# Kernel optimization log

Hardware: AMD Instinct MI355X
Metric: run time of the kernel (lower is better)

Reference implementation:

```python
import jax, jax.numpy as jnp
import numpy as np

N_HEAD = 16
MA_K = 0.02          # sigmoid temperature in ma_k_activation
LEAKY_SLOPE = 0.02   # negative_slope in ma_q_activation
NEG_INF = -1e9


def setup_inputs() -> dict:
    key = jax.random.key(0)
    k1, k2, k3, k4 = jax.random.split(key, 4)
    B, T, C = 2, 2048, 1024
    x = jax.random.normal(k1, (B, T, C), dtype=jnp.float32)
    s = 1.0 / np.sqrt(C)
    W_attn = jax.random.normal(k2, (C, 2 * C), dtype=jnp.float32) * s
    W_k2 = jax.random.normal(k3, (C, C), dtype=jnp.float32) * s
    W_proj = jax.random.normal(k4, (C, C), dtype=jnp.float32) * s
    return {"x": x, "W_attn": W_attn, "W_k2": W_k2, "W_proj": W_proj}


def _heads(t, H):
    # [B,T,C] -> [B,H,T,d]
    B, T, C = t.shape
    return t.reshape(B, T, H, C // H).transpose(0, 2, 1, 3)


def reference(x, W_attn, W_k2, W_proj):
    B, T, C = x.shape
    H = N_HEAD
    d = C // H
    scale = 1.0 / jnp.sqrt(jnp.asarray(d, x.dtype))

    qk = x @ W_attn                      # [B,T,2C]
    q, k = jnp.split(qk, 2, axis=-1)
    q = _heads(q, H)                     # [B,H,T,d]
    k = _heads(k, H)
    v = _heads(x, H)                     # v = x

    # --- AR branch: causal softmax attention ---
    scores = jnp.einsum('bhtd,bhsd->bhts', q, k) * scale
    causal = jnp.tril(jnp.ones((T, T), dtype=bool))
    scores = jnp.where(causal, scores, NEG_INF)
    attn = jax.nn.softmax(scores, axis=-1)
    y = jnp.einsum('bhts,bhsd->bhtd', attn, v)   # [B,H,T,d]

    # --- MA branch: causal, softmax-free linear attention on residual ---
    e = v[:, :, 1:, :] - y[:, :, :-1, :]          # [B,H,T-1,d]
    k2 = _heads(x[:, :-1, :] @ W_k2, H)           # [B,H,T-1,d]
    q2 = q[:, :, 1:, :]                           # [B,H,T-1,d]

    qa = -jax.nn.leaky_relu(-q2 * scale, negative_slope=LEAKY_SLOPE)
    ka = jax.nn.sigmoid(MA_K * (k2 * scale))

    w = jnp.einsum('bhtd,bhsd->bhts', qa, ka)     # [B,H,T-1,T-1]
    w = jnp.tril(w)
    y2 = jnp.einsum('bhts,bhsd->bhtd', w, e)      # [B,H,T-1,d]
    y2 = jnp.concatenate([jnp.zeros_like(y2[:, :, :1, :]), y2], axis=2)  # pad front

    def merge(t):  # [B,H,T,d] -> [B,T,C]
        return t.transpose(0, 2, 1, 3).reshape(B, T, C)

    return merge(y) @ W_proj + merge(y2) @ W_proj
```

## Files before the change

### kernel.cpp

```cpp
#include <hip/hip_runtime.h>

typedef unsigned short u16;
typedef u16   u16x4  __attribute__((ext_vector_type(4)));
typedef u16   u16x8  __attribute__((ext_vector_type(8)));
typedef __bf16 bf16x8 __attribute__((ext_vector_type(8)));
typedef float  f32x4  __attribute__((ext_vector_type(4)));

__device__ __forceinline__ float bf2f(u16 v) {
    unsigned u = ((unsigned)v) << 16;
    return __builtin_bit_cast(float, u);
}
__device__ __forceinline__ u16 f2bf(float f) {
    unsigned u = __builtin_bit_cast(unsigned, f);
    u += 0x7fffu + ((u >> 16) & 1u);
    return (u16)(u >> 16);
}

__device__ __forceinline__ size_t kimg_idx(int bh, int s, int d) {
    return ((size_t)(bh * 32 + (s >> 6)) * 4096) + (size_t)(((d >> 3) * 64 + (s & 63)) * 8) + (d & 7);
}
__device__ __forceinline__ size_t vimg_idx(int bh, int s, int d) {
    return ((size_t)(bh * 32 + (s >> 6)) * 4096) + (size_t)((((s & 63) >> 3) * 64 + d) * 8) + (s & 7);
}

__global__ __launch_bounds__(256)
void convert_pack(const float* __restrict__ in, u16* __restrict__ xb,
                  u16* __restrict__ xpack) {
    int i = blockIdx.x * 256 + threadIdx.x;
    int c4 = i & 255, row = i >> 8;
    int s = row & 2047, b = row >> 11;
    float4 v = ((const float4*)in)[i];
    u16x4 o;
    o.x = f2bf(v.x); o.y = f2bf(v.y); o.z = f2bf(v.z); o.w = f2bf(v.w);
    ((u16x4*)xb)[i] = o;
    int h = c4 >> 4, d0 = (c4 & 15) * 4;
    size_t base = vimg_idx(b * 16 + h, s, d0);
    xpack[base]      = o.x;
    xpack[base + 8]  = o.y;
    xpack[base + 16] = o.z;
    xpack[base + 24] = o.w;
}

__global__ __launch_bounds__(256)
void transpose_f32_bf16(const float* __restrict__ in, u16* __restrict__ out,
                        int R, int Cd) {
    __shared__ u16 tile[64][65];
    const int c0 = blockIdx.x * 64, r0 = blockIdx.y * 64;
    const int tid = threadIdx.x;
#pragma unroll
    for (int i = 0; i < 16; ++i) {
        int idx = tid + i * 256;
        int r = idx >> 6, c = idx & 63;
        tile[r][c] = f2bf(in[(size_t)(r0 + r) * Cd + c0 + c]);
    }
    __syncthreads();
#pragma unroll
    for (int i = 0; i < 16; ++i) {
        int idx = tid + i * 256;
        int r = idx >> 6, c = idx & 63;
        out[(size_t)(c0 + r) * R + r0 + c] = tile[c][r];
    }
}

__global__ __launch_bounds__(256, 2)
void gemm_qk(const u16* __restrict__ A, const u16* __restrict__ Bt,
             u16* __restrict__ qs, u16* __restrict__ kpack, int K) {
    __shared__ __align__(16) u16 As[4][128][8];
    __shared__ __align__(16) u16 Bs[4][128][8];
    const int tid = threadIdx.x;
    const int wave = tid >> 6, lane = tid & 63;
    const int m0 = blockIdx.y * 128, n0 = blockIdx.x * 128;
    const int wm = (wave >> 1) * 64, wn = (wave & 1) * 64;
    const int q = lane >> 4, mr = lane & 15;
    const int sr = tid >> 2, c8 = tid & 3;
    const u16* Ap = A + (size_t)(m0 + sr) * K + c8 * 8;
    const u16* Bp = Bt + (size_t)(n0 + sr) * K + c8 * 8;

    f32x4 acc[4][4];
#pragma unroll
    for (int i = 0; i < 4; ++i)
#pragma unroll
        for (int j = 0; j < 4; ++j) acc[i][j] = f32x4{0.f, 0.f, 0.f, 0.f};

    u16x8 a0, a1, b0, b1;
    auto gload = [&](int k0) {
        a0 = *(const u16x8*)(Ap + k0);
        a1 = *(const u16x8*)(Ap + k0 + (size_t)64 * K);
        b0 = *(const u16x8*)(Bp + k0);
        b1 = *(const u16x8*)(Bp + k0 + (size_t)64 * K);
    };
    gload(0);
    for (int k0 = 0; k0 < K; k0 += 32) {
        __syncthreads();
        *(u16x8*)&As[c8][sr][0]      = a0;
        *(u16x8*)&As[c8][sr + 64][0] = a1;
        *(u16x8*)&Bs[c8][sr][0]      = b0;
        *(u16x8*)&Bs[c8][sr + 64][0] = b1;
        __syncthreads();
        if (k0 + 32 < K) gload(k0 + 32);
        bf16x8 af[4], bfr[4];
#pragma unroll
        for (int i = 0; i < 4; ++i) af[i]  = *(const bf16x8*)&As[q][wm + i * 16 + mr][0];
#pragma unroll
        for (int j = 0; j < 4; ++j) bfr[j] = *(const bf16x8*)&Bs[q][wn + j * 16 + mr][0];
#pragma unroll
        for (int i = 0; i < 4; ++i)
#pragma unroll
            for (int j = 0; j < 4; ++j)
                acc[i][j] = __builtin_amdgcn_mfma_f32_16x16x32_bf16(af[i], bfr[j], acc[i][j], 0, 0, 0);
    }
#pragma unroll
    for (int i = 0; i < 4; ++i)
#pragma unroll
        for (int j = 0; j < 4; ++j)
#pragma unroll
            for (int r = 0; r < 4; ++r) {
                int m = m0 + wm + i * 16 + q * 4 + r;
                int n = n0 + wn + j * 16 + mr;
                float v = acc[i][j][r];
                if (n < 1024) {
                    qs[(size_t)m * 1024 + n] = f2bf(v * 0.125f);
                } else {
                    int b = m >> 11, s = m & 2047, nn = n - 1024;
                    kpack[kimg_idx(b * 16 + (nn >> 6), s, nn & 63)] = f2bf(v);
                }
            }
}

template <int EPI>
__global__ __launch_bounds__(256, 2)
void gemm64(const u16* __restrict__ A, const u16* __restrict__ Bt,
            void* __restrict__ Cv, int N, int K) {
    __shared__ __align__(16) u16 As[4][64][8];
    __shared__ __align__(16) u16 Bs[4][128][8];
    const int tid = threadIdx.x;
    const int wave = tid >> 6, lane = tid & 63;
    const int m0 = blockIdx.y * 64, n0 = blockIdx.x * 128;
    const int wn0 = wave * 32;
    const int q = lane >> 4, mr = lane & 15;
    const int sr = tid >> 2, c8 = tid & 3;
    const u16* Ap = A + (size_t)(m0 + sr) * K + c8 * 8;
    const u16* Bp = Bt + (size_t)(n0 + sr) * K + c8 * 8;

    f32x4 acc[4][2];
#pragma unroll
    for (int i = 0; i < 4; ++i)
#pragma unroll
        for (int j = 0; j < 2; ++j) acc[i][j] = f32x4{0.f, 0.f, 0.f, 0.f};

    u16x8 a0, b0, b1;
    auto gload = [&](int k0) {
        a0 = *(const u16x8*)(Ap + k0);
        b0 = *(const u16x8*)(Bp + k0);
        b1 = *(const u16x8*)(Bp + k0 + (size_t)64 * K);
    };
    gload(0);
    for (int k0 = 0; k0 < K; k0 += 32) {
        __syncthreads();
        *(u16x8*)&As[c8][sr][0]      = a0;
        *(u16x8*)&Bs[c8][sr][0]      = b0;
        *(u16x8*)&Bs[c8][sr + 64][0] = b1;
        __syncthreads();
        if (k0 + 32 < K) gload(k0 + 32);
        bf16x8 af[4], bfr[2];
#pragma unroll
        for (int i = 0; i < 4; ++i) af[i]  = *(const bf16x8*)&As[q][i * 16 + mr][0];
#pragma unroll
        for (int j = 0; j < 2; ++j) bfr[j] = *(const bf16x8*)&Bs[q][wn0 + j * 16 + mr][0];
#pragma unroll
        for (int i = 0; i < 4; ++i)
#pragma unroll
            for (int j = 0; j < 2; ++j)
                acc[i][j] = __builtin_amdgcn_mfma_f32_16x16x32_bf16(af[i], bfr[j], acc[i][j], 0, 0, 0);
    }
#pragma unroll
    for (int i = 0; i < 4; ++i)
#pragma unroll
        for (int j = 0; j < 2; ++j)
#pragma unroll
            for (int r = 0; r < 4; ++r) {
                int m = m0 + i * 16 + q * 4 + r;
                int n = n0 + wn0 + j * 16 + mr;
                float v = acc[i][j][r];
                if (EPI == 1) {
                    ((float*)Cv)[(size_t)m * N + n] = v;
                } else {
                    int b = m >> 11, s = m & 2047;
                    ((u16*)Cv)[kimg_idx(b * 16 + (n >> 6), s, n & 63)] =
                        f2bf(1.f / (1.f + __expf(-0.0025f * v)));
                }
            }
}

__global__ __launch_bounds__(256, 4)
void flash_mfma(const u16* __restrict__ qs, const u16* __restrict__ kpack,
                const u16* __restrict__ xpack, u16* __restrict__ Opart,
                float* __restrict__ lpart) {
    __shared__ __align__(16) u16 Ks[8][64][8];
    __shared__ __align__(16) u16 Vs[8][64][8];
    __shared__ __align__(16) u16 Ps[4][16][72];
    const int bh = blockIdx.y, b = bh >> 4, hc = (bh & 15) * 64;
    const int z = blockIdx.z;
    const int tid = threadIdx.x, w = tid >> 6, lane = tid & 63;
    const int n16 = lane & 15, quad = lane >> 4;
    const u16* kbase = kpack + (size_t)bh * 32 * 4096;
    const u16* vbase = xpack + (size_t)bh * 32 * 4096;
    u16* Ob = Opart + (size_t)z * 4096 * 1024;
    float* lb = lpart + z * 65536;

    for (int rep = 0; rep < 2; ++rep) {
        const int tile = rep ? 31 - (int)blockIdx.x : (int)blockIdx.x;
        const int t0 = tile * 64;
        const int nchunk = tile + 1;

        bf16x8 qf[2];
        {
            const int trow = t0 + w * 16 + n16;
            const u16* qp = &qs[(size_t)(b * 2048 + trow) * 1024 + hc + quad * 8];
            qf[0] = *(const bf16x8*)qp;
            qf[1] = *(const bf16x8*)(qp + 32);
        }

        f32x4 O[4];
        float lsum[4];
#pragma unroll
        for (int jt = 0; jt < 4; ++jt) O[jt] = f32x4{0.f, 0.f, 0.f, 0.f};
#pragma unroll
        for (int r = 0; r < 4; ++r) lsum[r] = 0.f;

        u16x8 kr0, kr1, vr0, vr1;
        auto pref = [&](int c) {
            const u16* kc = kbase + (size_t)c * 4096;
            const u16* vc = vbase + (size_t)c * 4096;
            kr0 = *(const u16x8*)(kc + tid * 8);
            kr1 = *(const u16x8*)(kc + (256 + tid) * 8);
            vr0 = *(const u16x8*)(vc + tid * 8);
            vr1 = *(const u16x8*)(vc + (256 + tid) * 8);
        };
        if (z < nchunk) pref(z);

        for (int c = z; c < nchunk; c += 2) {
            __syncthreads();
            *(u16x8*)((u16*)Ks + tid * 8)         = kr0;
            *(u16x8*)((u16*)Ks + (256 + tid) * 8) = kr1;
            *(u16x8*)((u16*)Vs + tid * 8)         = vr0;
            *(u16x8*)((u16*)Vs + (256 + tid) * 8) = vr1;
            __syncthreads();
            if (c + 2 < nchunk) pref(c + 2);

            f32x4 S[4];
#pragma unroll
            for (int jt = 0; jt < 4; ++jt) S[jt] = f32x4{0.f, 0.f, 0.f, 0.f};
#pragma unroll
            for (int ks = 0; ks < 2; ++ks)
#pragma unroll
                for (int jt = 0; jt < 4; ++jt) {
                    bf16x8 kf = *(const bf16x8*)&Ks[ks * 4 + quad][jt * 16 + n16][0];
                    S[jt] = __builtin_amdgcn_mfma_f32_16x16x32_bf16(qf[ks], kf, S[jt], 0, 0, 0);
                }

            float p[4][4];
#pragma unroll
            for (int reg = 0; reg < 4; ++reg)
#pragma unroll
                for (int jt = 0; jt < 4; ++jt)
                    p[reg][jt] = __expf(S[jt][reg] - 16.0f);
            if (c == tile) {
#pragma unroll
                for (int reg = 0; reg < 4; ++reg) {
                    const int tr = w * 16 + quad * 4 + reg;
#pragma unroll
                    for (int jt = 0; jt < 4; ++jt)
                        if (jt * 16 + n16 > tr) p[reg][jt] = 0.f;
                }
            }
#pragma unroll
            for (int reg = 0; reg < 4; ++reg) {
                lsum[reg] += (p[reg][0] + p[reg][1]) + (p[reg][2] + p[reg][3]);
#pragma unroll
                for (int jt = 0; jt < 4; ++jt)
                    Ps[w][quad * 4 + reg][jt * 16 + n16] = f2bf(p[reg][jt]);
            }

            bf16x8 pf[2];
#pragma unroll
            for (int ks = 0; ks < 2; ++ks)
                pf[ks] = *(const bf16x8*)&Ps[w][n16][ks * 32 + quad * 8];
#pragma unroll
            for (int ks = 0; ks < 2; ++ks)
#pragma unroll
                for (int jt = 0; jt < 4; ++jt) {
                    bf16x8 vf = *(const bf16x8*)&Vs[ks * 4 + quad][jt * 16 + n16][0];
                    O[jt] = __builtin_amdgcn_mfma_f32_16x16x32_bf16(pf[ks], vf, O[jt], 0, 0, 0);
                }
        }

#pragma unroll
        for (int reg = 0; reg < 4; ++reg) {
            float l = lsum[reg];
#pragma unroll
            for (int off = 1; off < 16; off <<= 1) l += __shfl_xor(l, off, 64);
            const int tr = t0 + w * 16 + quad * 4 + reg;
            if (n16 == 0) lb[bh * 2048 + tr] = l;
            const size_t row = (size_t)(b * 2048 + tr) * 1024 + hc;
#pragma unroll
            for (int jt = 0; jt < 4; ++jt)
                Ob[row + jt * 16 + n16] = f2bf(O[jt][reg]);
        }
    }
}

__global__ __launch_bounds__(256)
void combine_flash(const u16* __restrict__ Opart, const float* __restrict__ lpart,
                   const u16* __restrict__ xb, u16* __restrict__ y,
                   u16* __restrict__ epack) {
    int i = blockIdx.x * 256 + threadIdx.x;
    int c4 = i & 255, row = i >> 8, t = row & 2047, b = row >> 11;
    int h = c4 >> 4, d0 = (c4 & 15) * 4;
    size_t off = (size_t)row * 1024 + c4 * 4;
    u16x4 o0 = *(const u16x4*)&Opart[off];
    u16x4 o1 = *(const u16x4*)&Opart[(size_t)4096 * 1024 + off];
    int lrow = (b * 16 + h) * 2048 + t;
    float inv = 1.f / (lpart[lrow] + lpart[65536 + lrow]);
    float y0 = (bf2f(o0.x) + bf2f(o1.x)) * inv;
    float y1 = (bf2f(o0.y) + bf2f(o1.y)) * inv;
    float y2 = (bf2f(o0.z) + bf2f(o1.z)) * inv;
    float y3 = (bf2f(o0.w) + bf2f(o1.w)) * inv;
    u16x4 yo;
    yo.x = f2bf(y0); yo.y = f2bf(y1); yo.z = f2bf(y2); yo.w = f2bf(y3);
    *(u16x4*)&y[off] = yo;
    float e0 = 0.f, e1 = 0.f, e2 = 0.f, e3 = 0.f;
    if (t < 2047) {
        u16x4 xv = *(const u16x4*)&xb[off + 1024];
        e0 = bf2f(xv.x) - y0; e1 = bf2f(xv.y) - y1;
        e2 = bf2f(xv.z) - y2; e3 = bf2f(xv.w) - y3;
    }
    size_t base = vimg_idx(b * 16 + h, t, d0);
    epack[base]      = f2bf(e0);
    epack[base + 8]  = f2bf(e1);
    epack[base + 16] = f2bf(e2);
    epack[base + 24] = f2bf(e3);
}

__global__ __launch_bounds__(256, 4)
void arma_mfma(const u16* __restrict__ qs, const u16* __restrict__ kapack,
               const u16* __restrict__ epack, u16* __restrict__ Opart) {
    __shared__ __align__(16) u16 Ks[8][64][8];
    __shared__ __align__(16) u16 Es[8][64][8];
    __shared__ __align__(16) u16 Ps[4][16][72];
    const int bh = blockIdx.y, b = bh >> 4, hc = (bh & 15) * 64;
    const int z = blockIdx.z;
    const int tid = threadIdx.x, w = tid >> 6, lane = tid & 63;
    const int n16 = lane & 15, quad = lane >> 4;
    const u16* kbase = kapack + (size_t)bh * 32 * 4096;
    const u16* vbase = epack + (size_t)bh * 32 * 4096;
    u16* Ob = Opart + (size_t)z * 4096 * 1024;

    for (int rep = 0; rep < 2; ++rep) {
        const int tile = rep ? 31 - (int)blockIdx.x : (int)blockIdx.x;
        const int t0 = tile * 64;
        const int nchunk = tile + 1;

        bf16x8 qf[2];
        {
            const int trow = t0 + w * 16 + n16;
            const u16* qp = &qs[(size_t)(b * 2048 + trow) * 1024 + hc + quad * 8];
#pragma unroll
            for (int ks = 0; ks < 2; ++ks) {
                u16x8 qv = *(const u16x8*)(qp + ks * 32);
                u16x8 o;
#pragma unroll
                for (int j = 0; j < 8; ++j) {
                    float zv = bf2f(qv[j]);
                    o[j] = f2bf(zv < 0.f ? zv : 0.02f * zv);
                }
                qf[ks] = __builtin_bit_cast(bf16x8, o);
            }
        }

        f32x4 O[4];
#pragma unroll
        for (int jt = 0; jt < 4; ++jt) O[jt] = f32x4{0.f, 0.f, 0.f, 0.f};

        u16x8 kr0, kr1, vr0, vr1;
        auto pref = [&](int c) {
            const u16* kc = kbase + (size_t)c * 4096;
            const u16* vc = vbase + (size_t)c * 4096;
            kr0 = *(const u16x8*)(kc + tid * 8);
            kr1 = *(const u16x8*)(kc + (256 + tid) * 8);
            vr0 = *(const u16x8*)(vc + tid * 8);
            vr1 = *(const u16x8*)(vc + (256 + tid) * 8);
        };
        if (z < nchunk) pref(z);

        for (int c = z; c < nchunk; c += 2) {
            __syncthreads();
            *(u16x8*)((u16*)Ks + tid * 8)         = kr0;
            *(u16x8*)((u16*)Ks + (256 + tid) * 8) = kr1;
            *(u16x8*)((u16*)Es + tid * 8)         = vr0;
            *(u16x8*)((u16*)Es + (256 + tid) * 8) = vr1;
            __syncthreads();
            if (c + 2 < nchunk) pref(c + 2);

            f32x4 S[4];
#pragma unroll
            for (int jt = 0; jt < 4; ++jt) S[jt] = f32x4{0.f, 0.f, 0.f, 0.f};
#pragma unroll
            for (int ks = 0; ks < 2; ++ks)
#pragma unroll
                for (int jt = 0; jt < 4; ++jt) {
                    bf16x8 kf = *(const bf16x8*)&Ks[ks * 4 + quad][jt * 16 + n16][0];
                    S[jt] = __builtin_amdgcn_mfma_f32_16x16x32_bf16(qf[ks], kf, S[jt], 0, 0, 0);
                }

            if (c == tile) {
#pragma unroll
                for (int reg = 0; reg < 4; ++reg) {
                    const int tr = w * 16 + quad * 4 + reg;
#pragma unroll
                    for (int jt = 0; jt < 4; ++jt)
                        if (jt * 16 + n16 >= tr) S[jt][reg] = 0.f;
                }
            }
#pragma unroll
            for (int reg = 0; reg < 4; ++reg)
#pragma unroll
                for (int jt = 0; jt < 4; ++jt)
                    Ps[w][quad * 4 + reg][jt * 16 + n16] = f2bf(S[jt][reg]);

            bf16x8 pf[2];
#pragma unroll
            for (int ks = 0; ks < 2; ++ks)
                pf[ks] = *(const bf16x8*)&Ps[w][n16][ks * 32 + quad * 8];
#pragma unroll
            for (int ks = 0; ks < 2; ++ks)
#pragma unroll
                for (int jt = 0; jt < 4; ++jt) {
                    bf16x8 ef = *(const bf16x8*)&Es[ks * 4 + quad][jt * 16 + n16][0];
                    O[jt] = __builtin_amdgcn_mfma_f32_16x16x32_bf16(pf[ks], ef, O[jt], 0, 0, 0);
                }
        }

#pragma unroll
        for (int reg = 0; reg < 4; ++reg) {
            const int tr = t0 + w * 16 + quad * 4 + reg;
            const size_t row = (size_t)(b * 2048 + tr) * 1024 + hc;
#pragma unroll
            for (int jt = 0; jt < 4; ++jt)
                Ob[row + jt * 16 + n16] = f2bf(O[jt][reg]);
        }
    }
}

__global__ __launch_bounds__(256)
void combine_arma(const u16* __restrict__ Opart, const u16* __restrict__ y,
                  u16* __restrict__ ys) {
    int i = blockIdx.x * 256 + threadIdx.x;
    size_t off = (size_t)i * 4;
    u16x4 o0 = *(const u16x4*)&Opart[off];
    u16x4 o1 = *(const u16x4*)&Opart[(size_t)4096 * 1024 + off];
    u16x4 yv = *(const u16x4*)&y[off];
    u16x4 r;
    r.x = f2bf(bf2f(yv.x) + bf2f(o0.x) + bf2f(o1.x));
    r.y = f2bf(bf2f(yv.y) + bf2f(o0.y) + bf2f(o1.y));
    r.z = f2bf(bf2f(yv.z) + bf2f(o0.z) + bf2f(o1.z));
    r.w = f2bf(bf2f(yv.w) + bf2f(o0.w) + bf2f(o1.w));
    *(u16x4*)&ys[off] = r;
}

extern "C" void kernel_launch(void* const* d_in, const int* in_sizes, int n_in,
                              void* d_out, int out_size, void* d_ws, size_t ws_size,
                              hipStream_t stream) {
    const float* x      = (const float*)d_in[0];
    const float* W_attn = (const float*)d_in[1];
    const float* W_k2   = (const float*)d_in[2];
    const float* W_proj = (const float*)d_in[3];
    float* out = (float*)d_out;

    char* w = (char*)d_ws;
    u16* xb      = (u16*)w; w += (size_t)4096 * 1024 * 2;
    u16* Wt_attn = (u16*)w; w += (size_t)2048 * 1024 * 2;
    u16* Wt_k2   = (u16*)w; w += (size_t)1024 * 1024 * 2;
    u16* Wt_proj = (u16*)w; w += (size_t)1024 * 1024 * 2;
    u16* qs      = (u16*)w; w += (size_t)4096 * 1024 * 2;
    u16* kpack   = (u16*)w; w += (size_t)4096 * 1024 * 2;
    u16* kapack  = (u16*)w; w += (size_t)4096 * 1024 * 2;
    u16* xpack   = (u16*)w; w += (size_t)4096 * 1024 * 2;
    u16* y       = (u16*)w; w += (size_t)4096 * 1024 * 2;
    u16* epack   = (u16*)w; w += (size_t)4096 * 1024 * 2;
    u16* Opart   = (u16*)w; w += (size_t)2 * 4096 * 1024 * 2;
    float* lpart = (float*)w; w += (size_t)2 * 65536 * 4;
    u16* ys = xb;

    convert_pack<<<dim3(4096), dim3(256), 0, stream>>>(x, xb, xpack);
    transpose_f32_bf16<<<dim3(32, 16), dim3(256), 0, stream>>>(W_attn, Wt_attn, 1024, 2048);
    transpose_f32_bf16<<<dim3(16, 16), dim3(256), 0, stream>>>(W_k2,   Wt_k2,   1024, 1024);
    transpose_f32_bf16<<<dim3(16, 16), dim3(256), 0, stream>>>(W_proj, Wt_proj, 1024, 1024);
    gemm_qk<<<dim3(16, 32), dim3(256), 0, stream>>>(xb, Wt_attn, qs, kpack, 1024);
    gemm64<2><<<dim3(8, 64), dim3(256), 0, stream>>>(xb, Wt_k2, kapack, 1024, 1024);
    flash_mfma<<<dim3(16, 32, 2), dim3(256), 0, stream>>>(qs, kpack, xpack, Opart, lpart);
    combine_flash<<<dim3(4096), dim3(256), 0, stream>>>(Opart, lpart, xb, y, epack);
    arma_mfma<<<dim3(16, 32, 2), dim3(256), 0, stream>>>(qs, kapack, epack, Opart);
    combine_arma<<<dim3(4096), dim3(256), 0, stream>>>(Opart, y, ys);
    gemm64<1><<<dim3(8, 64), dim3(256), 0, stream>>>(ys, Wt_proj, out, 1024, 1024);
}
```

Baseline: 307.8 us.

## Double query rows per attention block to reuse staged K/V tiles

The causal flash and ARMA attention kernels now give each block 128 query rows instead of 64, with two 16-row m-tiles per wave. Each K/V (or K/E) chunk staged in LDS is reused for twice as many rows, the V fragments are loaded once per chunk, and the grid is halved with launch bounds lowered to 2 blocks per CU. The three weight-transpose launches are merged into a single launch that picks its weight by block index. In exchange, fewer blocks are resident, registers per thread go up, and the fixed exp offset of 16 is dropped from the softmax, which changes how close the exponent runs to overflow.

```diff
diff --git a/kernel.cpp b/kernel.cpp
--- a/kernel.cpp
+++ b/kernel.cpp
@@ -42,10 +42,16 @@
 }
 
 __global__ __launch_bounds__(256)
-void transpose_f32_bf16(const float* __restrict__ in, u16* __restrict__ out,
-                        int R, int Cd) {
+void prep_weights(const float* __restrict__ Wa, const float* __restrict__ Wk,
+                  const float* __restrict__ Wp, u16* __restrict__ Wta,
+                  u16* __restrict__ Wtk, u16* __restrict__ Wtp) {
     __shared__ u16 tile[64][65];
-    const int c0 = blockIdx.x * 64, r0 = blockIdx.y * 64;
+    const int bx = blockIdx.x;
+    const float* in; u16* out; int Cd, cx;
+    if (bx < 32)      { in = Wa; out = Wta; Cd = 2048; cx = bx; }
+    else if (bx < 48) { in = Wk; out = Wtk; Cd = 1024; cx = bx - 32; }
+    else              { in = Wp; out = Wtp; Cd = 1024; cx = bx - 48; }
+    const int c0 = cx * 64, r0 = blockIdx.y * 64;
     const int tid = threadIdx.x;
 #pragma unroll
     for (int i = 0; i < 16; ++i) {
@@ -58,7 +64,7 @@
     for (int i = 0; i < 16; ++i) {
         int idx = tid + i * 256;
         int r = idx >> 6, c = idx & 63;
-        out[(size_t)(c0 + r) * R + r0 + c] = tile[c][r];
+        out[(size_t)(c0 + r) * 1024 + r0 + c] = tile[c][r];
     }
 }
 
@@ -192,7 +198,7 @@
             }
 }
 
-__global__ __launch_bounds__(256, 4)
+__global__ __launch_bounds__(256, 2)
 void flash_mfma(const u16* __restrict__ qs, const u16* __restrict__ kpack,
                 const u16* __restrict__ xpack, u16* __restrict__ Opart,
                 float* __restrict__ lpart) {
@@ -209,24 +215,29 @@
     float* lb = lpart + z * 65536;
 
     for (int rep = 0; rep < 2; ++rep) {
-        const int tile = rep ? 31 - (int)blockIdx.x : (int)blockIdx.x;
-        const int t0 = tile * 64;
-        const int nchunk = tile + 1;
-
-        bf16x8 qf[2];
-        {
-            const int trow = t0 + w * 16 + n16;
+        const int T = rep ? 15 - (int)blockIdx.x : (int)blockIdx.x;
+        const int t0 = T * 128;
+        const int nchunk = 2 * T + 2;
+
+        bf16x8 qf[2][2];
+#pragma unroll
+        for (int mt = 0; mt < 2; ++mt) {
+            const int trow = t0 + (w + mt * 4) * 16 + n16;
             const u16* qp = &qs[(size_t)(b * 2048 + trow) * 1024 + hc + quad * 8];
-            qf[0] = *(const bf16x8*)qp;
-            qf[1] = *(const bf16x8*)(qp + 32);
+            qf[mt][0] = *(const bf16x8*)qp;
+            qf[mt][1] = *(const bf16x8*)(qp + 32);
         }
 
-        f32x4 O[4];
-        float lsum[4];
-#pragma unroll
-        for (int jt = 0; jt < 4; ++jt) O[jt] = f32x4{0.f, 0.f, 0.f, 0.f};
-#pragma unroll
-        for (int r = 0; r < 4; ++r) lsum[r] = 0.f;
+        f32x4 O[2][4];
+        float lsum[2][4];
+#pragma unroll
+        for (int mt = 0; mt < 2; ++mt)
+#pragma unroll
+            for (int jt = 0; jt < 4; ++jt) { O[mt][jt] = f32x4{0.f, 0.f, 0.f, 0.f}; }
+#pragma unroll
+        for (int mt = 0; mt < 2; ++mt)
+#pragma unroll
+            for (int r = 0; r < 4; ++r) lsum[mt][r] = 0.f;
 
         u16x8 kr0, kr1, vr0, vr1;
         auto pref = [&](int c) {
@@ -248,65 +259,76 @@
             __syncthreads();
             if (c + 2 < nchunk) pref(c + 2);
 
-            f32x4 S[4];
-#pragma unroll
-            for (int jt = 0; jt < 4; ++jt) S[jt] = f32x4{0.f, 0.f, 0.f, 0.f};
+            f32x4 S[2][4];
+#pragma unroll
+            for (int mt = 0; mt < 2; ++mt)
+#pragma unroll
+                for (int jt = 0; jt < 4; ++jt) S[mt][jt] = f32x4{0.f, 0.f, 0.f, 0.f};
 #pragma unroll
             for (int ks = 0; ks < 2; ++ks)
 #pragma unroll
                 for (int jt = 0; jt < 4; ++jt) {
                     bf16x8 kf = *(const bf16x8*)&Ks[ks * 4 + quad][jt * 16 + n16][0];
-                    S[jt] = __builtin_amdgcn_mfma_f32_16x16x32_bf16(qf[ks], kf, S[jt], 0, 0, 0);
-                }
-
-            float p[4][4];
-#pragma unroll
-            for (int reg = 0; reg < 4; ++reg)
+                    S[0][jt] = __builtin_amdgcn_mfma_f32_16x16x32_bf16(qf[0][ks], kf, S[0][jt], 0, 0, 0);
+                    S[1][jt] = __builtin_amdgcn_mfma_f32_16x16x32_bf16(qf[1][ks], kf, S[1][jt], 0, 0, 0);
+                }
+            bf16x8 vf[2][4];
+#pragma unroll
+            for (int ks = 0; ks < 2; ++ks)
 #pragma unroll
                 for (int jt = 0; jt < 4; ++jt)
-                    p[reg][jt] = __expf(S[jt][reg] - 16.0f);
-            if (c == tile) {
+                    vf[ks][jt] = *(const bf16x8*)&Vs[ks * 4 + quad][jt * 16 + n16][0];
+
+            const int mt0 = (c == 2 * T + 1) ? 1 : 0;
+            for (int mt = mt0; mt < 2; ++mt) {
+                float p[4][4];
+#pragma unroll
+                for (int reg = 0; reg < 4; ++reg)
+#pragma unroll
+                    for (int jt = 0; jt < 4; ++jt)
+                        p[reg][jt] = __expf(S[mt][jt][reg]);
+                if (c == 2 * T + mt) {
+#pragma unroll
+                    for (int reg = 0; reg < 4; ++reg) {
+                        const int tr = t0 + (w + mt * 4) * 16 + quad * 4 + reg;
+#pragma unroll
+                        for (int jt = 0; jt < 4; ++jt)
+                            if (c * 64 + jt * 16 + n16 > tr) p[reg][jt] = 0.f;
+                    }
+                }
 #pragma unroll
                 for (int reg = 0; reg < 4; ++reg) {
-                    const int tr = w * 16 + quad * 4 + reg;
+                    lsum[mt][reg] += (p[reg][0] + p[reg][1]) + (p[reg][2] + p[reg][3]);
 #pragma unroll
                     for (int jt = 0; jt < 4; ++jt)
-                        if (jt * 16 + n16 > tr) p[reg][jt] = 0.f;
-                }
-            }
+                        Ps[w][quad * 4 + reg][jt * 16 + n16] = f2bf(p[reg][jt]);
+                }
+                bf16x8 pf[2];
+#pragma unroll
+                for (int ks = 0; ks < 2; ++ks)
+                    pf[ks] = *(const bf16x8*)&Ps[w][n16][ks * 32 + quad * 8];
+#pragma unroll
+                for (int ks = 0; ks < 2; ++ks)
+#pragma unroll
+                    for (int jt = 0; jt < 4; ++jt)
+                        O[mt][jt] = __builtin_amdgcn_mfma_f32_16x16x32_bf16(pf[ks], vf[ks][jt], O[mt][jt], 0, 0, 0);
+            }
+        }
+
+#pragma unroll
+        for (int mt = 0; mt < 2; ++mt)
 #pragma unroll
             for (int reg = 0; reg < 4; ++reg) {
-                lsum[reg] += (p[reg][0] + p[reg][1]) + (p[reg][2] + p[reg][3]);
+                float l = lsum[mt][reg];
+#pragma unroll
+                for (int off = 1; off < 16; off <<= 1) l += __shfl_xor(l, off, 64);
+                const int tr = t0 + (w + mt * 4) * 16 + quad * 4 + reg;
+                if (n16 == 0) lb[bh * 2048 + tr] = l;
+                const size_t row = (size_t)(b * 2048 + tr) * 1024 + hc;
 #pragma unroll
                 for (int jt = 0; jt < 4; ++jt)
-                    Ps[w][quad * 4 + reg][jt * 16 + n16] = f2bf(p[reg][jt]);
-            }
-
-            bf16x8 pf[2];
-#pragma unroll
-            for (int ks = 0; ks < 2; ++ks)
-                pf[ks] = *(const bf16x8*)&Ps[w][n16][ks * 32 + quad * 8];
-#pragma unroll
-            for (int ks = 0; ks < 2; ++ks)
-#pragma unroll
-                for (int jt = 0; jt < 4; ++jt) {
-                    bf16x8 vf = *(const bf16x8*)&Vs[ks * 4 + quad][jt * 16 + n16][0];
-                    O[jt] = __builtin_amdgcn_mfma_f32_16x16x32_bf16(pf[ks], vf, O[jt], 0, 0, 0);
-                }
-        }
-
-#pragma unroll
-        for (int reg = 0; reg < 4; ++reg) {
-            float l = lsum[reg];
-#pragma unroll
-            for (int off = 1; off < 16; off <<= 1) l += __shfl_xor(l, off, 64);
-            const int tr = t0 + w * 16 + quad * 4 + reg;
-            if (n16 == 0) lb[bh * 2048 + tr] = l;
-            const size_t row = (size_t)(b * 2048 + tr) * 1024 + hc;
-#pragma unroll
-            for (int jt = 0; jt < 4; ++jt)
-                Ob[row + jt * 16 + n16] = f2bf(O[jt][reg]);
-        }
+                    Ob[row + jt * 16 + n16] = f2bf(O[mt][jt][reg]);
+            }
     }
 }
 
@@ -342,7 +364,7 @@
     epack[base + 24] = f2bf(e3);
 }
 
-__global__ __launch_bounds__(256, 4)
+__global__ __launch_bounds__(256, 2)
 void arma_mfma(const u16* __restrict__ qs, const u16* __restrict__ kapack,
                const u16* __restrict__ epack, u16* __restrict__ Opart) {
     __shared__ __align__(16) u16 Ks[8][64][8];
@@ -357,13 +379,14 @@
     u16* Ob = Opart + (size_t)z * 4096 * 1024;
 
     for (int rep = 0; rep < 2; ++rep) {
-        const int tile = rep ? 31 - (int)blockIdx.x : (int)blockIdx.x;
-        const int t0 = tile * 64;
-        const int nchunk = tile + 1;
-
-        bf16x8 qf[2];
-        {
-            const int trow = t0 + w * 16 + n16;
+        const int T = rep ? 15 - (int)blockIdx.x : (int)blockIdx.x;
+        const int t0 = T * 128;
+        const int nchunk = 2 * T + 2;
+
+        bf16x8 qf[2][2];
+#pragma unroll
+        for (int mt = 0; mt < 2; ++mt) {
+            const int trow = t0 + (w + mt * 4) * 16 + n16;
             const u16* qp = &qs[(size_t)(b * 2048 + trow) * 1024 + hc + quad * 8];
 #pragma unroll
             for (int ks = 0; ks < 2; ++ks) {
@@ -374,13 +397,15 @@
                     float zv = bf2f(qv[j]);
                     o[j] = f2bf(zv < 0.f ? zv : 0.02f * zv);
                 }
-                qf[ks] = __builtin_bit_cast(bf16x8, o);
+                qf[mt][ks] = __builtin_bit_cast(bf16x8, o);
             }
         }
 
-        f32x4 O[4];
-#pragma unroll
-        for (int jt = 0; jt < 4; ++jt) O[jt] = f32x4{0.f, 0.f, 0.f, 0.f};
+        f32x4 O[2][4];
+#pragma unroll
+        for (int mt = 0; mt < 2; ++mt)
+#pragma unroll
+            for (int jt = 0; jt < 4; ++jt) O[mt][jt] = f32x4{0.f, 0.f, 0.f, 0.f};
 
         u16x8 kr0, kr1, vr0, vr1;
         auto pref = [&](int c) {
@@ -402,53 +427,64 @@
             __syncthreads();
             if (c + 2 < nchunk) pref(c + 2);
 
-            f32x4 S[4];
-#pragma unroll
-            for (int jt = 0; jt < 4; ++jt) S[jt] = f32x4{0.f, 0.f, 0.f, 0.f};
+            f32x4 S[2][4];
+#pragma unroll
+            for (int mt = 0; mt < 2; ++mt)
+#pragma unroll
+                for (int jt = 0; jt < 4; ++jt) S[mt][jt] = f32x4{0.f, 0.f, 0.f, 0.f};
 #pragma unroll
             for (int ks = 0; ks < 2; ++ks)
 #pragma unroll
                 for (int jt = 0; jt < 4; ++jt) {
                     bf16x8 kf = *(const bf16x8*)&Ks[ks * 4 + quad][jt * 16 + n16][0];
-                    S[jt] = __builtin_amdgcn_mfma_f32_16x16x32_bf16(qf[ks], kf, S[jt], 0, 0, 0);
-                }
-
-            if (c == tile) {
-#pragma unroll
-                for (int reg = 0; reg < 4; ++reg) {
-                    const int tr = w * 16 + quad * 4 + reg;
+                    S[0][jt] = __builtin_amdgcn_mfma_f32_16x16x32_bf16(qf[0][ks], kf, S[0][jt], 0, 0, 0);
+                    S[1][jt] = __builtin_amdgcn_mfma_f32_16x16x32_bf16(qf[1][ks], kf, S[1][jt], 0, 0, 0);
+                }
+            bf16x8 vf[2][4];
+#pragma unroll
+            for (int ks = 0; ks < 2; ++ks)
+#pragma unroll
+                for (int jt = 0; jt < 4; ++jt)
+                    vf[ks][jt] = *(const bf16x8*)&Es[ks * 4 + quad][jt * 16 + n16][0];
+
+            const int mt0 = (c == 2 * T + 1) ? 1 : 0;
+            for (int mt = mt0; mt < 2; ++mt) {
+                if (c == 2 * T + mt) {
+#pragma unroll
+                    for (int reg = 0; reg < 4; ++reg) {
+                        const int tr = t0 + (w + mt * 4) * 16 + quad * 4 + reg;
+#pragma unroll
+                        for (int jt = 0; jt < 4; ++jt)
+                            if (c * 64 + jt * 16 + n16 >= tr) S[mt][jt][reg] = 0.f;
+                    }
+                }
+#pragma unroll
+                for (int reg = 0; reg < 4; ++reg)
 #pragma unroll
                     for (int jt = 0; jt < 4; ++jt)
-                        if (jt * 16 + n16 >= tr) S[jt][reg] = 0.f;
-                }
-            }
-#pragma unroll
-            for (int reg = 0; reg < 4; ++reg)
+                        Ps[w][quad * 4 + reg][jt * 16 + n16] = f2bf(S[mt][jt][reg]);
+                bf16x8 pf[2];
+#pragma unroll
+                for (int ks = 0; ks < 2; ++ks)
+                    pf[ks] = *(const bf16x8*)&Ps[w][n16][ks * 32 + quad * 8];
+#pragma unroll
+                for (int ks = 0; ks < 2; ++ks)
+#pragma unroll
+                    for (int jt = 0; jt < 4; ++jt)
+                        O[mt][jt] = __builtin_amdgcn_mfma_f32_16x16x32_bf16(pf[ks], vf[ks][jt], O[mt][jt], 0, 0, 0);
+            }
+        }
+
+#pragma unroll
+        for (int mt = 0; mt < 2; ++mt)
+#pragma unroll
+            for (int reg = 0; reg < 4; ++reg) {
+                const int tr = t0 + (w + mt * 4) * 16 + quad * 4 + reg;
+                const size_t row = (size_t)(b * 2048 + tr) * 1024 + hc;
 #pragma unroll
                 for (int jt = 0; jt < 4; ++jt)
-                    Ps[w][quad * 4 + reg][jt * 16 + n16] = f2bf(S[jt][reg]);
-
-            bf16x8 pf[2];
-#pragma unroll
-            for (int ks = 0; ks < 2; ++ks)
-                pf[ks] = *(const bf16x8*)&Ps[w][n16][ks * 32 + quad * 8];
-#pragma unroll
-            for (int ks = 0; ks < 2; ++ks)
-#pragma unroll
-                for (int jt = 0; jt < 4; ++jt) {
-                    bf16x8 ef = *(const bf16x8*)&Es[ks * 4 + quad][jt * 16 + n16][0];
-                    O[jt] = __builtin_amdgcn_mfma_f32_16x16x32_bf16(pf[ks], ef, O[jt], 0, 0, 0);
-                }
-        }
-
-#pragma unroll
-        for (int reg = 0; reg < 4; ++reg) {
-            const int tr = t0 + w * 16 + quad * 4 + reg;
-            const size_t row = (size_t)(b * 2048 + tr) * 1024 + hc;
-#pragma unroll
-            for (int jt = 0; jt < 4; ++jt)
-                Ob[row + jt * 16 + n16] = f2bf(O[jt][reg]);
-        }
+                    Ob[row + jt * 16 + n16] = f2bf(O[mt][jt][reg]);
+            }
     }
 }
 
@@ -493,14 +529,13 @@
     u16* ys = xb;
 
     convert_pack<<<dim3(4096), dim3(256), 0, stream>>>(x, xb, xpack);
-    transpose_f32_bf16<<<dim3(32, 16), dim3(256), 0, stream>>>(W_attn, Wt_attn, 1024, 2048);
-    transpose_f32_bf16<<<dim3(16, 16), dim3(256), 0, stream>>>(W_k2,   Wt_k2,   1024, 1024);
-    transpose_f32_bf16<<<dim3(16, 16), dim3(256), 0, stream>>>(W_proj, Wt_proj, 1024, 1024);
+    prep_weights<<<dim3(64, 16), dim3(256), 0, stream>>>(W_attn, W_k2, W_proj,
+                                                         Wt_attn, Wt_k2, Wt_proj);
     gemm_qk<<<dim3(16, 32), dim3(256), 0, stream>>>(xb, Wt_attn, qs, kpack, 1024);
     gemm64<2><<<dim3(8, 64), dim3(256), 0, stream>>>(xb, Wt_k2, kapack, 1024, 1024);
-    flash_mfma<<<dim3(16, 32, 2), dim3(256), 0, stream>>>(qs, kpack, xpack, Opart, lpart);
+    flash_mfma<<<dim3(8, 32, 2), dim3(256), 0, stream>>>(qs, kpack, xpack, Opart, lpart);
     combine_flash<<<dim3(4096), dim3(256), 0, stream>>>(Opart, lpart, xb, y, epack);
-    arma_mfma<<<dim3(16, 32, 2), dim3(256), 0, stream>>>(qs, kapack, epack, Opart);
+    arma_mfma<<<dim3(8, 32, 2), dim3(256), 0, stream>>>(qs, kapack, epack, Opart);
     combine_arma<<<dim3(4096), dim3(256), 0, stream>>>(Opart, y, ys);
     gemm64<1><<<dim3(8, 64), dim3(256), 0, stream>>>(ys, Wt_proj, out, 1024, 1024);
 }
```

New measurement: 481.8 us. 56.5% more time.
